# Kernel optimization log

Hardware: AMD Instinct MI355X
Metric: run time of the kernel (lower is better)

## Reference

```python
import jax, jax.numpy as jnp
import numpy as np

T = 4096; D = 768; V = 32000; L = 4; EPS = 1e-5


def _ln(x, g, b):
    m = jnp.mean(x, axis=-1, keepdims=True)
    v = jnp.mean((x - m) ** 2, axis=-1, keepdims=True)
    return (x - m) * jax.lax.rsqrt(v + EPS) * g + b


def _qgelu(x):
    return x * jax.nn.sigmoid(1.702 * x)


def setup_inputs() -> dict:
    key = jax.random.key(0)
    ks = jax.random.split(key, 10)
    s = 0.02
    return {
        "idx": jax.random.randint(ks[0], (T,), 0, V),
        "wte": jax.random.normal(ks[1], (V, D)) * s,
        "rb_ln_g": jnp.ones((D,)), "rb_ln_b": jnp.zeros((D,)),
        "rb_fc_w": jax.random.normal(ks[2], (D, 4 * D)) * s,
        "rb_fc_b": jnp.zeros((4 * D,)),
        "rb_proj_w": jax.random.normal(ks[3], (4 * D, D)) * s,
        "rb_proj_b": jnp.zeros((D,)),
        "lnf_g": jnp.ones((D,)), "lnf_b": jnp.zeros((D,)),
        "lm_head_w": jax.random.normal(ks[4], (D, V)) * s,
        "mb_ln_g": jnp.ones((L, 2 * D)), "mb_ln_b": jnp.zeros((L, 2 * D)),
        "mb_fc_w": jax.random.normal(ks[5], (L, 2 * D, 4 * D)) * s,
        "mb_fc_b": jnp.zeros((L, 4 * D)),
        "mb_proj_w": jax.random.normal(ks[6], (L, 4 * D, D)) * s,
        "mb_proj_b": jnp.zeros((L, D)),
        "op_w": jax.random.normal(ks[7], (L, D, D)) * s,
        "op_b": jnp.zeros((L, D)),
        "lns_g": jnp.ones((L, D)), "lns_b": jnp.zeros((L, D)),
        "heads_w": jax.random.normal(ks[8], (L, D, V)) * s,
    }


def reference(idx, wte, rb_ln_g, rb_ln_b, rb_fc_w, rb_fc_b, rb_proj_w, rb_proj_b,
              lnf_g, lnf_b, lm_head_w, mb_ln_g, mb_ln_b, mb_fc_w, mb_fc_b,
              mb_proj_w, mb_proj_b, op_w, op_b, lns_g, lns_b, heads_w):
    # token embedding (dropout is identity in eval) + initial residual block
    x = wte[idx]  # [T, D]
    h = _ln(x, rb_ln_g, rb_ln_b)
    x = x + _qgelu(h @ rb_fc_w + rb_fc_b) @ rb_proj_w + rb_proj_b
    x = _ln(x, lnf_g, lnf_b)
    logits = x @ lm_head_w  # [T, V]

    # targets=None path: pred_targets = cat(idx[1:], [-1])
    pred_targets = jnp.concatenate([idx[1:], jnp.full((1,), -1, idx.dtype)])
    pos = jnp.arange(T)
    skey = jax.random.key(42)

    for i in range(L):  # static small loop over layers
        j = i + 1
        # multinomial(softmax(logits), 1) == categorical(logits)
        idx_next = jax.random.categorical(jax.random.fold_in(skey, i), logits)
        # positions p where the sample matched the next-token target and p < T - j
        mask = (idx_next == pred_targets) & (pos < T - j)  # [T] bool
        # x2[p] = x[p + j] (padded); compute merge densely, select with mask
        x2 = jnp.concatenate([x[j:], jnp.zeros((j, D), x.dtype)], axis=0)
        h = _ln(jnp.concatenate([x, x2], axis=-1), mb_ln_g[i], mb_ln_b[i])
        merged = x2 + _qgelu(h @ mb_fc_w[i] + mb_fc_b[i]) @ mb_proj_w[i] + mb_proj_b[i]
        # scatter merged[p] into x at position p + j where mask[p]
        merged_s = jnp.concatenate([jnp.zeros((j, D), x.dtype), merged[:-j]], axis=0)
        mask_s = jnp.concatenate([jnp.zeros((j,), bool), mask[:-j]], axis=0)
        x = jnp.where(mask_s[:, None], merged_s, x)
        x = x @ op_w[i] + op_b[i]
        x = _ln(x, lns_g[i], lns_b[i])
        logits = x @ heads_w[i]
    return logits
```

## Files before the change

### kernel.cpp

```cpp
#include <hip/hip_runtime.h>
#include <cstdint>
#include <cstddef>

#define T_TOK 4096
#define DIM   768
#define VOCAB 32000
#define NLAYER 4
#define HALF_TV 65536000u

typedef short bf16x8 __attribute__((ext_vector_type(8)));
typedef float f32x4  __attribute__((ext_vector_type(4)));
typedef float f32x4v __attribute__((ext_vector_type(4)));

__host__ __device__ inline void tf2x32(uint32_t k0, uint32_t k1, uint32_t& v0, uint32_t& v1){
  uint32_t ks2 = k0 ^ k1 ^ 0x1BD11BDAu;
  uint32_t x0 = v0 + k0, x1 = v1 + k1;
#define TFR(R) { x0 += x1; x1 = (x1<<R)|(x1>>(32-R)); x1 ^= x0; }
  TFR(13) TFR(15) TFR(26) TFR(6)
  x0 += k1;  x1 += ks2 + 1u;
  TFR(17) TFR(29) TFR(16) TFR(24)
  x0 += ks2; x1 += k0 + 2u;
  TFR(13) TFR(15) TFR(26) TFR(6)
  x0 += k0;  x1 += k1 + 3u;
  TFR(17) TFR(29) TFR(16) TFR(24)
  x0 += k1;  x1 += ks2 + 4u;
  TFR(13) TFR(15) TFR(26) TFR(6)
  x0 += ks2; x1 += k0 + 5u;
#undef TFR
  v0 = x0; v1 = x1;
}

__device__ inline float neglog_u(uint32_t k){
  float L;
  if (k >= 0x780000u){
    float x = (float)(0x800000u - k) * 1.1920928955078125e-7f;
    L = x * fmaf(x, fmaf(x, fmaf(x, 0.25f, 0.3333333333333f), 0.5f), 1.0f);
  } else {
    float l2k = __builtin_amdgcn_logf((float)k);
    L = 0.69314718055994531f * (23.0f - l2k);
    if (k == 0u) L = 87.33654475055310898f;
  }
  return L;
}

__device__ inline void gumbel_pair(uint32_t kf0, uint32_t kf1, uint32_t t_up, uint32_t v,
                                   float& gu, float& gd){
  uint32_t m = t_up * (uint32_t)VOCAB + v;
  uint32_t x0 = m, x1 = m + HALF_TV;
  tf2x32(kf0, kf1, x0, x1);
  float Lu = neglog_u(x0 >> 9);
  float Ld = neglog_u(x1 >> 9);
  gu = -0.69314718055994531f * __builtin_amdgcn_logf(Lu);
  gd = -0.69314718055994531f * __builtin_amdgcn_logf(Ld);
}

__device__ inline unsigned short f2bf(float f){
  uint32_t u = __float_as_uint(f);
  return (unsigned short)((u + 0x7FFFu + ((u >> 16) & 1u)) >> 16);
}
__device__ inline float bf2f(unsigned short h){
  return __uint_as_float(((uint32_t)h) << 16);
}
__device__ inline void cvt8(const float* f, bool lo, unsigned short* out){
  #pragma unroll
  for (int e=0;e<8;e++){
    float x = f[e];
    unsigned short h = f2bf(x);
    if (lo) h = f2bf(x - bf2f(h));
    out[e] = h;
  }
}
__device__ inline float blockReduceSum(float v){
  __shared__ float red[4];
  #pragma unroll
  for (int off=32; off>0; off>>=1) v += __shfl_down(v, off);
  int w = threadIdx.x >> 6;
  __syncthreads();
  if ((threadIdx.x & 63) == 0) red[w] = v;
  __syncthreads();
  return red[0] + red[1] + red[2] + red[3];
}

__device__ inline void gload16(const void* g, void* l){
  __builtin_amdgcn_global_load_lds(
      (const __attribute__((address_space(1))) unsigned int*)g,
      (__attribute__((address_space(3))) unsigned int*)l, 16, 0, 0);
}

enum { ST_F32 = 0, ST_HILO = 1, ST_SAMPLE = 2 };

template<int KSTEPS, int NSEG, int STORE, bool NTST>
__global__ __launch_bounds__(512) void k_hgemm256(
    const unsigned short* __restrict__ A0, const unsigned short* __restrict__ A1,
    const unsigned short* __restrict__ B0, const unsigned short* __restrict__ B2,
    float* __restrict__ C, uint32_t kf0, uint32_t kf1,
    unsigned long long* __restrict__ row_best, int N)
{
  constexpr int K  = KSTEPS * 64;
  constexpr int NT = NSEG * KSTEPS;
  __shared__ unsigned short sAll[65536];

  const int t = threadIdx.x;
  const int w = t >> 6, l = t & 63;
  const int wm = w >> 2, wn = w & 3;
  const int g = l >> 4, r = l & 15;
  const int lr = l >> 3, lc = l & 7;

  int bid = blockIdx.x;
  int xcd = bid & 7, c = bid >> 3;
  int bm = xcd*2 + (c & 1);
  int bn = c >> 1;

  f32x4 acc[8][4] = {};

  int grow[8];
  #pragma unroll
  for (int p=0;p<4;p++){
    int mr = p*64 + w*8 + lr;
    int blk = mr >> 4;
    grow[p] = (bm*128 + ((blk>>1)<<4) + (mr & 15) + ((blk & 1) ? 2048 : 0)) * K;
  }
  #pragma unroll
  for (int p=0;p<4;p++){
    int nr = p*64 + w*8 + lr;
    grow[4+p] = (bn*256 + nr) * K;
  }
  const int swz  = (lc ^ lr) << 3;
  const int ldst = w*1024 + l*16;

  auto stage = [&](int vt){
    char* base = (char*)sAll + (vt & 1) * 65536;
    int seg = (NSEG == 1) ? 0 : (vt / KSTEPS);
    int k0  = ((NSEG == 1) ? vt : (vt % KSTEPS)) * 64;
    const unsigned short* Ap = (seg == 1) ? A1 : A0;
    const unsigned short* Bp = (seg == 2) ? B2 : B0;
    #pragma unroll
    for (int p=0;p<4;p++)
      gload16(Ap + (size_t)(grow[p] + k0) + swz, base + p*8192 + ldst);
    #pragma unroll
    for (int p=0;p<4;p++)
      gload16(Bp + (size_t)(grow[4+p] + k0) + swz, base + 32768 + p*8192 + ldst);
  };

  stage(0);
  __syncthreads();

  for (int vt = 0; vt < NT; ++vt){
    if (vt + 1 < NT) stage(vt + 1);
    const char* sA = (const char*)sAll + (vt & 1) * 65536;
    const char* sB = sA + 32768;
    __builtin_amdgcn_s_setprio(1);
    #pragma unroll
    for (int kk=0;kk<2;kk++){
      bf16x8 bv[4];
      #pragma unroll
      for (int ni=0;ni<4;ni++){
        int tr = wn*64 + ni*16 + r;
        bv[ni] = *(const bf16x8*)(sB + tr*128 + (((kk*4+g) ^ (r&7))<<4));
      }
      #pragma unroll
      for (int mh=0; mh<2; mh++){
        bf16x8 av[4];
        #pragma unroll
        for (int q=0;q<4;q++){
          int tr = wm*128 + (mh*4+q)*16 + r;
          av[q] = *(const bf16x8*)(sA + tr*128 + (((kk*4+g) ^ (r&7))<<4));
        }
        #pragma unroll
        for (int q=0;q<4;q++)
          #pragma unroll
          for (int ni=0;ni<4;ni++)
            acc[mh*4+q][ni] = __builtin_amdgcn_mfma_f32_16x16x32_bf16(av[q], bv[ni], acc[mh*4+q][ni], 0, 0, 0);
      }
    }
    __builtin_amdgcn_s_setprio(0);
    __syncthreads();
  }

  if constexpr (STORE == ST_SAMPLE){
    #pragma unroll
    for (int mi=0; mi<8; mi+=2){
      int blk = wm*8 + mi;
      int row16 = (blk>>1) << 4;
      #pragma unroll
      for (int jj=0;jj<4;jj++){
        uint32_t t_up = bm*128 + row16 + g*4 + jj;
        unsigned long long bu = 0ull, bd = 0ull;
        #pragma unroll
        for (int ni=0;ni<4;ni++){
          uint32_t v = bn*256 + wn*64 + ni*16 + r;
          float gu, gd;
          gumbel_pair(kf0, kf1, t_up, v, gu, gd);
          float vu = acc[mi][ni][jj]   + gu;
          float vd = acc[mi+1][ni][jj] + gd;
          uint32_t fu = __float_as_uint(vu); fu = (fu & 0x80000000u) ? ~fu : (fu | 0x80000000u);
          uint32_t fd = __float_as_uint(vd); fd = (fd & 0x80000000u) ? ~fd : (fd | 0x80000000u);
          unsigned long long pu = ((unsigned long long)fu << 32) | (unsigned long long)(~v);
          unsigned long long pd = ((unsigned long long)fd << 32) | (unsigned long long)(~v);
          if (pu > bu) bu = pu;
          if (pd > bd) bd = pd;
        }
        #pragma unroll
        for (int off=1; off<16; off<<=1){
          unsigned int l0 = (unsigned int)bu, h0 = (unsigned int)(bu>>32);
          unsigned int l1 = __shfl_xor(l0, off), h1 = __shfl_xor(h0, off);
          unsigned long long o = ((unsigned long long)h1 << 32) | (unsigned long long)l1;
          if (o > bu) bu = o;
          l0 = (unsigned int)bd; h0 = (unsigned int)(bd>>32);
          l1 = __shfl_xor(l0, off); h1 = __shfl_xor(h0, off);
          o = ((unsigned long long)h1 << 32) | (unsigned long long)l1;
          if (o > bd) bd = o;
        }
        if (r == 0){
          atomicMax(&row_best[t_up], bu);
          atomicMax(&row_best[t_up + 2048], bd);
        }
      }
    }
  } else {
    #pragma unroll
    for (int mi=0;mi<8;mi++){
      int blk = wm*8 + mi;
      int mbase = bm*128 + ((blk>>1)<<4) + ((blk & 1) ? 2048 : 0);
      #pragma unroll
      for (int ni=0;ni<4;ni++){
        int n = bn*256 + wn*64 + ni*16 + r;
        #pragma unroll
        for (int jj=0;jj<4;jj++){
          int m = mbase + g*4 + jj;
          float v = acc[mi][ni][jj];
          if constexpr (NTST) __builtin_nontemporal_store(v, &C[(size_t)m * N + n]);
          else                C[(size_t)m * N + n] = v;
        }
      }
    }
  }
}

template<int KSTEPS, int NSEG, bool BIAS, bool QGELU, bool RES, int STORE>
__global__ __launch_bounds__(256) void k_hgemm(
    const unsigned short* __restrict__ A0, const unsigned short* __restrict__ A1,
    const unsigned short* __restrict__ B0, const unsigned short* __restrict__ B2,
    float* __restrict__ C, unsigned short* __restrict__ Ch, unsigned short* __restrict__ Cl,
    const float* __restrict__ bias, const float* __restrict__ res,
    int N, uint32_t kf0, uint32_t kf1, unsigned long long* __restrict__ row_best)
{
  constexpr int K = KSTEPS * 64;
  __shared__ unsigned short sA[128*64];
  __shared__ unsigned short sB[128*64];
  const int t = threadIdx.x;
  const int wave = t >> 6, lane = t & 63;
  const int wm = wave >> 1, wn = wave & 1;
  const int g = lane >> 4, r = lane & 15;
  const int lr = lane >> 3, lc = lane & 7;

  int bid = blockIdx.x;
  int xcd = bid & 7, c = bid >> 3;
  int bm = xcd*4 + (c & 3);
  int bn = c >> 2;

  f32x4 acc[4][4] = {};

  for (int kb = 0; kb < NSEG*KSTEPS; ++kb){
    const int seg = (NSEG == 1) ? 0 : (kb / KSTEPS);
    const int k0  = (NSEG == 1) ? kb*64 : (kb % KSTEPS) * 64;
    const unsigned short* Ap = (seg == 1) ? A1 : A0;
    const unsigned short* Bp = (seg == 2) ? B2 : B0;
    __syncthreads();
    #pragma unroll
    for (int p=0;p<4;p++){
      int mr = p*32 + wave*8 + lr;
      int blk = mr >> 4;
      int grow = bm*64 + ((blk>>1)<<4) + (mr & 15) + ((blk & 1) ? 2048 : 0);
      int gk = k0 + ((lc ^ lr) << 3);
      gload16(Ap + (size_t)grow * K + gk, (char*)sA + mr*128 + lc*16);
      int nrow = bn*128 + mr;
      gload16(Bp + (size_t)nrow * K + gk, (char*)sB + mr*128 + lc*16);
    }
    __syncthreads();
    #pragma unroll
    for (int kk=0;kk<2;kk++){
      bf16x8 av[4], bv[4];
      #pragma unroll
      for (int mi=0;mi<4;mi++){
        int tr = wm*64 + mi*16 + r;
        av[mi] = *(const bf16x8*)((const char*)sA + tr*128 + (((kk*4+g) ^ (r&7))<<4));
      }
      #pragma unroll
      for (int ni=0;ni<4;ni++){
        int tr = wn*64 + ni*16 + r;
        bv[ni] = *(const bf16x8*)((const char*)sB + tr*128 + (((kk*4+g) ^ (r&7))<<4));
      }
      #pragma unroll
      for (int mi=0;mi<4;mi++)
        #pragma unroll
        for (int ni=0;ni<4;ni++)
          acc[mi][ni] = __builtin_amdgcn_mfma_f32_16x16x32_bf16(av[mi], bv[ni], acc[mi][ni], 0, 0, 0);
    }
  }

  #pragma unroll
  for (int mi=0;mi<4;mi++){
    int blk2 = wm*4 + mi;
    int mbase = bm*64 + ((blk2>>1)<<4) + ((blk2 & 1) ? 2048 : 0);
    #pragma unroll
    for (int ni=0;ni<4;ni++){
      int n = bn*128 + wn*64 + ni*16 + r;
      float bv_ = BIAS ? bias[n] : 0.0f;
      #pragma unroll
      for (int jj=0;jj<4;jj++){
        int m = mbase + g*4 + jj;
        float v = acc[mi][ni][jj] + bv_;
        if constexpr (QGELU) v = v / (1.0f + expf(-1.702f * v));
        if constexpr (RES)   v += res[(size_t)m * N + n];
        if constexpr (STORE == ST_F32){
          C[(size_t)m * N + n] = v;
        } else {
          unsigned short h = f2bf(v);
          Ch[(size_t)m * N + n] = h;
          Cl[(size_t)m * N + n] = f2bf(v - bf2f(h));
        }
      }
    }
  }
}

template<bool SPLIT>
__global__ __launch_bounds__(256) void k_wt_t(const float* __restrict__ W,
    unsigned short* __restrict__ Bh, unsigned short* __restrict__ Bl, int K, int N)
{
  __shared__ unsigned short sH[64][72];
  __shared__ unsigned short sL[64][72];
  int kt = blockIdx.x, nt = blockIdx.y;
  int t = threadIdx.x;
  int kr = t >> 4, nc4 = (t & 15) * 4;
  #pragma unroll
  for (int p=0;p<4;p++){
    int k = p*16 + kr;
    f32x4v w = __builtin_nontemporal_load((const f32x4v*)&W[(size_t)(kt*64 + k) * N + nt*64 + nc4]);
    #pragma unroll
    for (int e=0;e<4;e++){
      unsigned short h = f2bf(w[e]);
      sH[nc4+e][k] = h;
      if (SPLIT) sL[nc4+e][k] = f2bf(w[e] - bf2f(h));
    }
  }
  __syncthreads();
  #pragma unroll
  for (int q=0;q<2;q++){
    int cid = t + q*256;
    int n = cid >> 3, ch = cid & 7;
    *(bf16x8*)&Bh[(size_t)(nt*64+n)*K + kt*64 + ch*8] = *(const bf16x8*)&sH[n][ch*8];
    if (SPLIT)
      *(bf16x8*)&Bl[(size_t)(nt*64+n)*K + kt*64 + ch*8] = *(const bf16x8*)&sL[n][ch*8];
  }
}

__global__ __launch_bounds__(256) void k_embed_ln(const int* __restrict__ idx,
    const float* __restrict__ wte, const float* __restrict__ g, const float* __restrict__ b,
    float* __restrict__ Xraw, unsigned short* __restrict__ Hh, unsigned short* __restrict__ Hl)
{
  int row = blockIdx.x;
  const float* src = wte + (size_t)idx[row] * DIM;
  float v[3];
  #pragma unroll
  for (int jj=0;jj<3;jj++) v[jj] = src[threadIdx.x + jj*256];
  float s = blockReduceSum(v[0]+v[1]+v[2]);
  float mean = s * (1.0f/DIM);
  float s2 = 0;
  #pragma unroll
  for (int jj=0;jj<3;jj++){ float d = v[jj]-mean; s2 += d*d; }
  s2 = blockReduceSum(s2);
  float rs = rsqrtf(s2 * (1.0f/DIM) + 1e-5f);
  #pragma unroll
  for (int jj=0;jj<3;jj++){
    int d = threadIdx.x + jj*256;
    Xraw[(size_t)row*DIM + d] = v[jj];
    float o = (v[jj]-mean)*rs*g[d] + b[d];
    unsigned short h = f2bf(o);
    Hh[(size_t)row*DIM + d] = h;
    Hl[(size_t)row*DIM + d] = f2bf(o - bf2f(h));
  }
}

__global__ __launch_bounds__(256) void k_ln(const float* __restrict__ in, float* __restrict__ out,
    const float* __restrict__ g, const float* __restrict__ b,
    unsigned short* __restrict__ obf, unsigned short* __restrict__ olo)
{
  int row = blockIdx.x;
  const float* src = in + (size_t)row * DIM;
  float v[3];
  #pragma unroll
  for (int jj=0;jj<3;jj++) v[jj] = src[threadIdx.x + jj*256];
  float s = blockReduceSum(v[0]+v[1]+v[2]);
  float mean = s * (1.0f/DIM);
  float s2 = 0;
  #pragma unroll
  for (int jj=0;jj<3;jj++){ float d = v[jj]-mean; s2 += d*d; }
  s2 = blockReduceSum(s2);
  float rs = rsqrtf(s2 * (1.0f/DIM) + 1e-5f);
  #pragma unroll
  for (int jj=0;jj<3;jj++){
    int d = threadIdx.x + jj*256;
    float o = (v[jj]-mean)*rs*g[d] + b[d];
    out[(size_t)row*DIM + d] = o;
    unsigned short h = f2bf(o);
    obf[(size_t)row*DIM + d] = h;
    olo[(size_t)row*DIM + d] = f2bf(o - bf2f(h));
  }
}

__global__ void k_mask(const unsigned long long* __restrict__ row_best,
    const int* __restrict__ idx, int j, int* __restrict__ count, int* __restrict__ plist)
{
  int t = blockIdx.x * blockDim.x + threadIdx.x;
  if (t >= T_TOK) return;
  int v = (int)(~(uint32_t)(row_best[t] & 0xFFFFFFFFull));
  int tgt = (t < T_TOK-1) ? idx[t+1] : -1;
  if (v == tgt && t < T_TOK - j){
    int pos = atomicAdd(count, 1);
    plist[pos] = t;
  }
}

__global__ __launch_bounds__(256) void k_merge(const float* __restrict__ X,
    const int* __restrict__ plist, const int* __restrict__ count,
    const float* __restrict__ lng, const float* __restrict__ lnb,
    const float* __restrict__ fcw, const float* __restrict__ fcb,
    const float* __restrict__ pjw, const float* __restrict__ pjb,
    float* __restrict__ mergebuf, int j)
{
  __shared__ float sh[1536 + 3072];
  int nb = *count;
  for (int bIdx = blockIdx.x; bIdx < nb; bIdx += gridDim.x){
    int p = plist[bIdx];
    const float* xp = X + (size_t)p * DIM;
    const float* x2 = X + (size_t)(p + j) * DIM;
    for (int d = threadIdx.x; d < 1536; d += 256)
      sh[d] = (d < DIM) ? xp[d] : x2[d - DIM];
    __syncthreads();
    float s = 0;
    for (int d = threadIdx.x; d < 1536; d += 256) s += sh[d];
    s = blockReduceSum(s);
    float mean = s * (1.0f/1536.0f);
    float s2 = 0;
    for (int d = threadIdx.x; d < 1536; d += 256){ float df = sh[d]-mean; s2 += df*df; }
    s2 = blockReduceSum(s2);
    float rs = rsqrtf(s2 * (1.0f/1536.0f) + 1e-5f);
    __syncthreads();
    for (int d = threadIdx.x; d < 1536; d += 256)
      sh[d] = (sh[d]-mean)*rs*lng[d] + lnb[d];
    __syncthreads();
    float* act = sh + 1536;
    #pragma unroll
    for (int jj=0;jj<12;jj++){
      int n = threadIdx.x + jj*256;
      float a = fcb[n];
      for (int k=0;k<1536;k++) a += sh[k]*fcw[(size_t)k*3072 + n];
      act[n] = a / (1.0f + expf(-1.702f*a));
    }
    __syncthreads();
    #pragma unroll
    for (int jj=0;jj<3;jj++){
      int d = threadIdx.x + jj*256;
      float a = pjb[d];
      for (int k=0;k<3072;k++) a += act[k]*pjw[(size_t)k*DIM + d];
      mergebuf[(size_t)bIdx*DIM + d] = x2[d] + a;
    }
    __syncthreads();
  }
}

__global__ void k_scatter(float* __restrict__ X, unsigned short* __restrict__ Xbf,
    unsigned short* __restrict__ Xlo, const float* __restrict__ mergebuf,
    const int* __restrict__ plist, const int* __restrict__ count, int j)
{
  int nb = *count;
  for (int bIdx = blockIdx.x; bIdx < nb; bIdx += gridDim.x){
    int p = plist[bIdx];
    for (int d = threadIdx.x; d < DIM; d += 256){
      float v = mergebuf[(size_t)bIdx*DIM + d];
      size_t o = (size_t)(p + j)*DIM + d;
      X[o] = v;
      unsigned short h = f2bf(v);
      Xbf[o] = h;
      Xlo[o] = f2bf(v - bf2f(h));
    }
  }
}

__global__ __launch_bounds__(256) void k_gemm_old(
    const float* __restrict__ A, const float* __restrict__ B, float* __restrict__ C,
    int M, int N, int K)
{
  __shared__ unsigned short sA[128*64];
  __shared__ unsigned short sB[128*64];
  const int t = threadIdx.x;
  const int bn = blockIdx.x, bm = blockIdx.y;
  const int wave = t >> 6, lane = t & 63;
  const int wm = wave >> 1, wn = wave & 1;
  const int g = lane >> 4, r = lane & 15;
  f32x4 acc[4][4] = {};
  const int nK = K >> 6;
  const int aC = t & 7,  aM0 = t >> 3;
  const int bN0 = t & 31, bC = t >> 5;
  const float* Abase = A + (size_t)(bm*128) * K;
  const float* Bbase = B + (size_t)(bn*128);
  for (int seg = 0; seg < 3; ++seg) {
    const bool aLO = (seg == 1), bLO = (seg == 2);
    for (int kb = 0; kb < nK; ++kb) {
      const int k0 = kb << 6;
      __syncthreads();
      #pragma unroll
      for (int p=0;p<4;p++){
        int m = p*32 + aM0;
        const float* src = Abase + (size_t)m * K + k0 + aC*8;
        float ff[8];
        *(float4*)(ff)   = *(const float4*)(src);
        *(float4*)(ff+4) = *(const float4*)(src+4);
        unsigned short hh[8];
        cvt8(ff, aLO, hh);
        *(bf16x8*)&sA[m*64 + ((aC ^ (m & 7)) * 8)] = *(bf16x8*)hh;
      }
      #pragma unroll
      for (int p=0;p<4;p++){
        int n = p*32 + bN0;
        float ff[8];
        const float* src = Bbase + (size_t)(k0 + bC*8) * N + n;
        #pragma unroll
        for (int e=0;e<8;e++) ff[e] = src[(size_t)e * N];
        unsigned short hh[8];
        cvt8(ff, bLO, hh);
        *(bf16x8*)&sB[n*64 + ((bC ^ (n & 7)) * 8)] = *(bf16x8*)hh;
      }
      __syncthreads();
      #pragma unroll
      for (int kk=0;kk<2;kk++){
        bf16x8 av[4], bv[4];
        #pragma unroll
        for (int mi=0;mi<4;mi++){
          int m = wm*64 + mi*16 + r;
          av[mi] = *(const bf16x8*)&sA[m*64 + (((kk*4 + g) ^ (m & 7)) * 8)];
        }
        #pragma unroll
        for (int ni=0;ni<4;ni++){
          int n = wn*64 + ni*16 + r;
          bv[ni] = *(const bf16x8*)&sB[n*64 + (((kk*4 + g) ^ (n & 7)) * 8)];
        }
        #pragma unroll
        for (int mi=0;mi<4;mi++)
          #pragma unroll
          for (int ni=0;ni<4;ni++)
            acc[mi][ni] = __builtin_amdgcn_mfma_f32_16x16x32_bf16(av[mi], bv[ni], acc[mi][ni], 0, 0, 0);
      }
    }
  }
  #pragma unroll
  for (int mi=0;mi<4;mi++)
    #pragma unroll
    for (int ni=0;ni<4;ni++)
      #pragma unroll
      for (int jj=0;jj<4;jj++){
        int m = bm*128 + wm*64 + mi*16 + g*4 + jj;
        int n = bn*128 + wn*64 + ni*16 + r;
        C[(size_t)m * N + n] = acc[mi][ni][jj];
      }
}

static void fold_key(uint32_t i, uint32_t& o0, uint32_t& o1){
  uint32_t x0 = 0, x1 = i;
  tf2x32(0u, 42u, x0, x1);
  o0 = x0; o1 = x1;
}

extern "C" void kernel_launch(void* const* d_in, const int* in_sizes, int n_in,
                              void* d_out, int out_size, void* d_ws, size_t ws_size,
                              hipStream_t stream)
{
  const int*   idx       = (const int*)  d_in[0];
  const float* wte       = (const float*)d_in[1];
  const float* rb_ln_g   = (const float*)d_in[2];
  const float* rb_ln_b   = (const float*)d_in[3];
  const float* rb_fc_w   = (const float*)d_in[4];
  const float* rb_fc_b   = (const float*)d_in[5];
  const float* rb_proj_w = (const float*)d_in[6];
  const float* rb_proj_b = (const float*)d_in[7];
  const float* lnf_g     = (const float*)d_in[8];
  const float* lnf_b     = (const float*)d_in[9];
  const float* lm_head_w = (const float*)d_in[10];
  const float* mb_ln_g   = (const float*)d_in[11];
  const float* mb_ln_b   = (const float*)d_in[12];
  const float* mb_fc_w   = (const float*)d_in[13];
  const float* mb_fc_b   = (const float*)d_in[14];
  const float* mb_proj_w = (const float*)d_in[15];
  const float* mb_proj_b = (const float*)d_in[16];
  const float* op_w      = (const float*)d_in[17];
  const float* op_b      = (const float*)d_in[18];
  const float* lns_g     = (const float*)d_in[19];
  const float* lns_b     = (const float*)d_in[20];
  const float* heads_w   = (const float*)d_in[21];

  const size_t TD = (size_t)T_TOK * DIM;
  const size_t DV = (size_t)DIM * VOCAB;

  float* X = (float*)d_ws;
  float* Y = X + TD;
  unsigned short* Xbf = (unsigned short*)(Y + TD);
  unsigned short* Xlo = Xbf + TD;
  unsigned short* BtFh = Xlo + TD;
  unsigned short* BtFl = BtFh + DV;
  size_t need_big = (size_t)((char*)(BtFl + DV) - (char*)d_ws);
  bool big = ws_size >= need_big;

  char* ob = (char*)d_out;
  float* OUT = (float*)d_out;
  unsigned short* Hh     = (unsigned short*)(ob);
  unsigned short* Hl     = Hh + TD;
  unsigned short* ACTh   = (unsigned short*)(ob + ((size_t)16<<20));
  unsigned short* ACTl   = ACTh + TD*4;
  unsigned short* Btfc_h = (unsigned short*)(ob + ((size_t)72<<20));
  unsigned short* Btfc_l = Btfc_h + (size_t)3072*DIM;
  unsigned short* Btpj_h = (unsigned short*)(ob + ((size_t)84<<20));
  unsigned short* Btpj_l = Btpj_h + (size_t)3072*DIM;
  unsigned short* BtS    = (unsigned short*)(ob + ((size_t)96<<20));
  unsigned short* Btop_h = (unsigned short*)(ob + ((size_t)152<<20));
  unsigned short* Btop_l = Btop_h + (size_t)DIM*DIM;
  float* MERGE = (float*)(ob + ((size_t)160<<20));
  unsigned long long* ROWBEST = (unsigned long long*)(ob + ((size_t)176<<20));
  int* PLIST = (int*)(ROWBEST + T_TOK);
  int* COUNT = PLIST + T_TOK;

  dim3 blk(256);
  dim3 blk8(512);

  k_embed_ln<<<T_TOK, blk, 0, stream>>>(idx, wte, rb_ln_g, rb_ln_b, X, Hh, Hl);
  k_wt_t<true><<<dim3(12,48), blk, 0, stream>>>(rb_fc_w,   Btfc_h, Btfc_l, DIM,  3072);
  k_wt_t<true><<<dim3(48,12), blk, 0, stream>>>(rb_proj_w, Btpj_h, Btpj_l, 3072, DIM);
  k_hgemm<12,3,true,true,false,ST_HILO><<<24*32, blk, 0, stream>>>(
      Hh, Hl, Btfc_h, Btfc_l, nullptr, ACTh, ACTl, rb_fc_b, nullptr, 3072, 0u,0u, nullptr);
  k_hgemm<48,3,true,false,true,ST_F32><<<6*32, blk, 0, stream>>>(
      ACTh, ACTl, Btpj_h, Btpj_l, Y, nullptr, nullptr, rb_proj_b, X, DIM, 0u,0u, nullptr);
  k_ln<<<T_TOK, blk, 0, stream>>>(Y, X, lnf_g, lnf_b, Xbf, Xlo);

  for (int i = 0; i < NLAYER; ++i){
    int j = i + 1;
    uint32_t kf0, kf1; fold_key((uint32_t)i, kf0, kf1);

    hipMemsetAsync(ROWBEST, 0, (size_t)T_TOK*8, stream);
    hipMemsetAsync(COUNT, 0, 4, stream);

    const float* hw = (i == 0) ? lm_head_w : heads_w + (size_t)(i-1)*DV;
    k_wt_t<false><<<dim3(12,500), blk, 0, stream>>>(hw, BtS, nullptr, DIM, VOCAB);
    k_hgemm256<12,1,ST_SAMPLE,false><<<2000, blk8, 0, stream>>>(
        Xbf, Xbf, BtS, BtS, nullptr, kf0, kf1, ROWBEST, VOCAB);

    k_mask<<<T_TOK/256, blk, 0, stream>>>(ROWBEST, idx, j, COUNT, PLIST);
    k_merge<<<64, blk, 0, stream>>>(X, PLIST, COUNT,
        mb_ln_g + (size_t)i*1536, mb_ln_b + (size_t)i*1536,
        mb_fc_w + (size_t)i*1536*3072, mb_fc_b + (size_t)i*3072,
        mb_proj_w + (size_t)i*3072*DIM, mb_proj_b + (size_t)i*DIM, MERGE, j);
    k_scatter<<<64, blk, 0, stream>>>(X, Xbf, Xlo, MERGE, PLIST, COUNT, j);

    k_wt_t<true><<<dim3(12,12), blk, 0, stream>>>(op_w + (size_t)i*DIM*DIM, Btop_h, Btop_l, DIM, DIM);
    k_hgemm<12,3,true,false,false,ST_F32><<<6*32, blk, 0, stream>>>(
        Xbf, Xlo, Btop_h, Btop_l, Y, nullptr, nullptr, op_b + (size_t)i*DIM, nullptr,
        DIM, 0u,0u, nullptr);
    k_ln<<<T_TOK, blk, 0, stream>>>(Y, X, lns_g + (size_t)i*DIM, lns_b + (size_t)i*DIM, Xbf, Xlo);
  }

  if (big){
    k_wt_t<true><<<dim3(12,500), blk, 0, stream>>>(heads_w + (size_t)3*DV, BtFh, BtFl, DIM, VOCAB);
    k_hgemm256<12,3,ST_F32,true><<<2000, blk8, 0, stream>>>(
        Xbf, Xlo, BtFh, BtFl, OUT, 0u, 0u, nullptr, VOCAB);
  } else {
    k_gemm_old<<<dim3(VOCAB/128, T_TOK/128), blk, 0, stream>>>(
        X, heads_w + (size_t)3*DV, OUT, T_TOK, VOCAB, DIM);
  }
}
```

Measured before the change: 2.814 ms.

## Use 1024-thread 256x256 GEMM blocks and route residual FC GEMM through them

```diff
diff --git a/kernel.cpp b/kernel.cpp
--- a/kernel.cpp
+++ b/kernel.cpp
@@ -89,11 +89,12 @@
 
 enum { ST_F32 = 0, ST_HILO = 1, ST_SAMPLE = 2 };
 
-template<int KSTEPS, int NSEG, int STORE, bool NTST>
-__global__ __launch_bounds__(512) void k_hgemm256(
+template<int KSTEPS, int NSEG, int STORE, bool NTST, bool BIAS, bool QGELU>
+__global__ __launch_bounds__(1024, 4) void k_hgemm256(
     const unsigned short* __restrict__ A0, const unsigned short* __restrict__ A1,
     const unsigned short* __restrict__ B0, const unsigned short* __restrict__ B2,
-    float* __restrict__ C, uint32_t kf0, uint32_t kf1,
+    float* __restrict__ C, unsigned short* __restrict__ Ch, unsigned short* __restrict__ Cl,
+    const float* __restrict__ bias, uint32_t kf0, uint32_t kf1,
     unsigned long long* __restrict__ row_best, int N)
 {
   constexpr int K  = KSTEPS * 64;
@@ -104,29 +105,25 @@
   const int w = t >> 6, l = t & 63;
   const int wm = w >> 2, wn = w & 3;
   const int g = l >> 4, r = l & 15;
-  const int lr = l >> 3, lc = l & 7;
 
   int bid = blockIdx.x;
   int xcd = bid & 7, c = bid >> 3;
   int bm = xcd*2 + (c & 1);
   int bn = c >> 1;
 
-  f32x4 acc[8][4] = {};
-
-  int grow[8];
-  #pragma unroll
-  for (int p=0;p<4;p++){
-    int mr = p*64 + w*8 + lr;
+  f32x4 acc[4][4] = {};
+
+  size_t arow[2], brow[2];
+  #pragma unroll
+  for (int p=0;p<2;p++){
+    int mr = p*128 + (t >> 3);
     int blk = mr >> 4;
-    grow[p] = (bm*128 + ((blk>>1)<<4) + (mr & 15) + ((blk & 1) ? 2048 : 0)) * K;
-  }
-  #pragma unroll
-  for (int p=0;p<4;p++){
-    int nr = p*64 + w*8 + lr;
-    grow[4+p] = (bn*256 + nr) * K;
-  }
-  const int swz  = (lc ^ lr) << 3;
-  const int ldst = w*1024 + l*16;
+    arow[p] = (size_t)(bm*128 + ((blk>>1)<<4) + (mr & 15) + ((blk & 1) ? 2048 : 0)) * K;
+    int nr = p*128 + (t >> 3);
+    brow[p] = (size_t)(bn*256 + nr) * K;
+  }
+  const int swz  = ((t & 7) ^ ((t >> 3) & 7)) << 3;
+  const int ldst = t * 16;
 
   auto stage = [&](int vt){
     char* base = (char*)sAll + (vt & 1) * 65536;
@@ -135,11 +132,11 @@
     const unsigned short* Ap = (seg == 1) ? A1 : A0;
     const unsigned short* Bp = (seg == 2) ? B2 : B0;
     #pragma unroll
-    for (int p=0;p<4;p++)
-      gload16(Ap + (size_t)(grow[p] + k0) + swz, base + p*8192 + ldst);
-    #pragma unroll
-    for (int p=0;p<4;p++)
-      gload16(Bp + (size_t)(grow[4+p] + k0) + swz, base + 32768 + p*8192 + ldst);
+    for (int p=0;p<2;p++)
+      gload16(Ap + arow[p] + k0 + swz, base + p*16384 + ldst);
+    #pragma unroll
+    for (int p=0;p<2;p++)
+      gload16(Bp + brow[p] + k0 + swz, base + 32768 + p*16384 + ldst);
   };
 
   stage(0);
@@ -149,39 +146,34 @@
     if (vt + 1 < NT) stage(vt + 1);
     const char* sA = (const char*)sAll + (vt & 1) * 65536;
     const char* sB = sA + 32768;
-    __builtin_amdgcn_s_setprio(1);
     #pragma unroll
     for (int kk=0;kk<2;kk++){
-      bf16x8 bv[4];
+      bf16x8 bv[4], av[4];
       #pragma unroll
       for (int ni=0;ni<4;ni++){
         int tr = wn*64 + ni*16 + r;
         bv[ni] = *(const bf16x8*)(sB + tr*128 + (((kk*4+g) ^ (r&7))<<4));
       }
       #pragma unroll
-      for (int mh=0; mh<2; mh++){
-        bf16x8 av[4];
-        #pragma unroll
-        for (int q=0;q<4;q++){
-          int tr = wm*128 + (mh*4+q)*16 + r;
-          av[q] = *(const bf16x8*)(sA + tr*128 + (((kk*4+g) ^ (r&7))<<4));
-        }
-        #pragma unroll
-        for (int q=0;q<4;q++)
-          #pragma unroll
-          for (int ni=0;ni<4;ni++)
-            acc[mh*4+q][ni] = __builtin_amdgcn_mfma_f32_16x16x32_bf16(av[q], bv[ni], acc[mh*4+q][ni], 0, 0, 0);
-      }
-    }
-    __builtin_amdgcn_s_setprio(0);
+      for (int q=0;q<4;q++){
+        int tr = wm*64 + q*16 + r;
+        av[q] = *(const bf16x8*)(sA + tr*128 + (((kk*4+g) ^ (r&7))<<4));
+      }
+      __builtin_amdgcn_s_setprio(1);
+      #pragma unroll
+      for (int q=0;q<4;q++)
+        #pragma unroll
+        for (int ni=0;ni<4;ni++)
+          acc[q][ni] = __builtin_amdgcn_mfma_f32_16x16x32_bf16(av[q], bv[ni], acc[q][ni], 0, 0, 0);
+      __builtin_amdgcn_s_setprio(0);
+    }
     __syncthreads();
   }
 
   if constexpr (STORE == ST_SAMPLE){
     #pragma unroll
-    for (int mi=0; mi<8; mi+=2){
-      int blk = wm*8 + mi;
-      int row16 = (blk>>1) << 4;
+    for (int mi=0; mi<4; mi+=2){
+      int row16 = (wm*2 + (mi>>1)) * 16;
       #pragma unroll
       for (int jj=0;jj<4;jj++){
         uint32_t t_up = bm*128 + row16 + g*4 + jj;
@@ -219,18 +211,26 @@
     }
   } else {
     #pragma unroll
-    for (int mi=0;mi<8;mi++){
-      int blk = wm*8 + mi;
+    for (int mi=0;mi<4;mi++){
+      int blk = wm*4 + mi;
       int mbase = bm*128 + ((blk>>1)<<4) + ((blk & 1) ? 2048 : 0);
       #pragma unroll
       for (int ni=0;ni<4;ni++){
         int n = bn*256 + wn*64 + ni*16 + r;
+        float bv_ = BIAS ? bias[n] : 0.0f;
         #pragma unroll
         for (int jj=0;jj<4;jj++){
           int m = mbase + g*4 + jj;
-          float v = acc[mi][ni][jj];
-          if constexpr (NTST) __builtin_nontemporal_store(v, &C[(size_t)m * N + n]);
-          else                C[(size_t)m * N + n] = v;
+          float v = acc[mi][ni][jj] + bv_;
+          if constexpr (QGELU) v = v / (1.0f + expf(-1.702f * v));
+          if constexpr (STORE == ST_F32){
+            if constexpr (NTST) __builtin_nontemporal_store(v, &C[(size_t)m * N + n]);
+            else                C[(size_t)m * N + n] = v;
+          } else {
+            unsigned short h = f2bf(v);
+            Ch[(size_t)m * N + n] = h;
+            Cl[(size_t)m * N + n] = f2bf(v - bf2f(h));
+          }
         }
       }
     }
@@ -631,13 +631,13 @@
   int* COUNT = PLIST + T_TOK;
 
   dim3 blk(256);
-  dim3 blk8(512);
+  dim3 blk16(1024);
 
   k_embed_ln<<<T_TOK, blk, 0, stream>>>(idx, wte, rb_ln_g, rb_ln_b, X, Hh, Hl);
   k_wt_t<true><<<dim3(12,48), blk, 0, stream>>>(rb_fc_w,   Btfc_h, Btfc_l, DIM,  3072);
   k_wt_t<true><<<dim3(48,12), blk, 0, stream>>>(rb_proj_w, Btpj_h, Btpj_l, 3072, DIM);
-  k_hgemm<12,3,true,true,false,ST_HILO><<<24*32, blk, 0, stream>>>(
-      Hh, Hl, Btfc_h, Btfc_l, nullptr, ACTh, ACTl, rb_fc_b, nullptr, 3072, 0u,0u, nullptr);
+  k_hgemm256<12,3,ST_HILO,false,true,true><<<16*12, blk16, 0, stream>>>(
+      Hh, Hl, Btfc_h, Btfc_l, nullptr, ACTh, ACTl, rb_fc_b, 0u,0u, nullptr, 3072);
   k_hgemm<48,3,true,false,true,ST_F32><<<6*32, blk, 0, stream>>>(
       ACTh, ACTl, Btpj_h, Btpj_l, Y, nullptr, nullptr, rb_proj_b, X, DIM, 0u,0u, nullptr);
   k_ln<<<T_TOK, blk, 0, stream>>>(Y, X, lnf_g, lnf_b, Xbf, Xlo);
@@ -651,8 +651,8 @@
 
     const float* hw = (i == 0) ? lm_head_w : heads_w + (size_t)(i-1)*DV;
     k_wt_t<false><<<dim3(12,500), blk, 0, stream>>>(hw, BtS, nullptr, DIM, VOCAB);
-    k_hgemm256<12,1,ST_SAMPLE,false><<<2000, blk8, 0, stream>>>(
-        Xbf, Xbf, BtS, BtS, nullptr, kf0, kf1, ROWBEST, VOCAB);
+    k_hgemm256<12,1,ST_SAMPLE,false,false,false><<<2000, blk16, 0, stream>>>(
+        Xbf, Xbf, BtS, BtS, nullptr, nullptr, nullptr, nullptr, kf0, kf1, ROWBEST, VOCAB);
 
     k_mask<<<T_TOK/256, blk, 0, stream>>>(ROWBEST, idx, j, COUNT, PLIST);
     k_merge<<<64, blk, 0, stream>>>(X, PLIST, COUNT,
@@ -670,8 +670,8 @@
 
   if (big){
     k_wt_t<true><<<dim3(12,500), blk, 0, stream>>>(heads_w + (size_t)3*DV, BtFh, BtFl, DIM, VOCAB);
-    k_hgemm256<12,3,ST_F32,true><<<2000, blk8, 0, stream>>>(
-        Xbf, Xlo, BtFh, BtFl, OUT, 0u, 0u, nullptr, VOCAB);
+    k_hgemm256<12,3,ST_F32,true,false,false><<<2000, blk16, 0, stream>>>(
+        Xbf, Xlo, BtFh, BtFl, OUT, nullptr, nullptr, nullptr, 0u, 0u, nullptr, VOCAB);
   } else {
     k_gemm_old<<<dim3(VOCAB/128, T_TOK/128), blk, 0, stream>>>(
         X, heads_w + (size_t)3*DV, OUT, T_TOK, VOCAB, DIM);
```

New measurement: 2.642 ms. 1.07x faster.
